# Kernel tuning notes

Measured on AMD Instinct MI355X. Metric: run time of the kernel, lower is better.

The kernel has to match this reference:

```python
import jax, jax.numpy as jnp
import numpy as np

SFREQ = 250.0
L_FREQ, H_FREQ = 4.0, 8.0
N_TAPS = 413  # odd, zero-phase FIR


def _bandpass_fir(numtaps, lf, hf, sfreq):
    # Hamming-windowed sinc band-pass (firwin-style), matching MNE's fir_design='firwin' spirit
    n = np.arange(numtaps) - (numtaps - 1) / 2.0
    lp = lambda fc: (2.0 * fc / sfreq) * np.sinc(2.0 * fc / sfreq * n)
    h = (lp(hf) - lp(lf)) * np.hamming(numtaps)
    return h.astype(np.float32)


def setup_inputs() -> dict:
    key = jax.random.key(0)
    x = jax.random.normal(key, (64, 64, 10000), dtype=jnp.float32)
    h = jnp.asarray(_bandpass_fir(N_TAPS, L_FREQ, H_FREQ, SFREQ))
    return {"x": x, "h": h}


def reference(x, h):
    # x: [B, C, T], h: [n_h] FIR filter. Equivalent math to _overlap_add_filter:
    # reflect_limited padding + full linear FFT convolution + zero-phase crop.
    T = x.shape[-1]
    n_h = h.shape[0]
    n_edge = min(n_h, T) - 1
    # reflect_limited pad: 2*x[0] - x[n_edge:0:-1] (left), 2*x[-1] - x[-2:-n_edge-2:-1] (right)
    left = 2.0 * x[..., :1] - x[..., 1:n_edge + 1][..., ::-1]
    right = 2.0 * x[..., -1:] - x[..., -n_edge - 1:-1][..., ::-1]
    x_ext = jnp.concatenate([left, x, right], axis=-1)  # [B, C, T + 2*n_edge]
    n_x = T + 2 * n_edge
    n_full = n_x + n_h - 1
    n_fft = 1 << (n_full - 1).bit_length()  # single big FFT == overlap-add result
    Xf = jnp.fft.rfft(x_ext, n_fft)
    Hf = jnp.fft.rfft(h.astype(x_ext.dtype), n_fft)
    y = jnp.fft.irfft(Xf * Hf, n_fft)  # full linear convolution of x_ext with h
    shift = (n_h - 1) // 2 + n_edge  # zero-phase delay compensation + edge crop
    return jax.lax.dynamic_slice_in_dim(y, shift, T, axis=-1).astype(x.dtype)
```

## Files before the change

kernel.cpp:

```cpp
#include <hip/hip_runtime.h>


#define T_LEN 10000
#define N_H   413
#define SHIFT 206
#define CB    512
#define BSPAN 3584
#define ROWH  936
#define NQ    28
#define AROWL 472

typedef _Float16 v8h   __attribute__((ext_vector_type(8)));
typedef float    v16f  __attribute__((ext_vector_type(16)));
typedef float    v4f   __attribute__((ext_vector_type(4)));
typedef float    f32x2 __attribute__((ext_vector_type(2)));

__device__ __forceinline__ void stage_load(const float* __restrict__ xr, int t0s,
                                           int jt, float sv[4][16]) {
    #pragma unroll
    for (int it = 0; it < 4; ++it) {
        const int c = jt + 16 * it;
        if (c < 58) {
            const int j0 = t0s + 16 * c;
            if (j0 >= SHIFT && j0 + 16 <= T_LEN + SHIFT) {
                const f32x2* xp = (const f32x2*)(xr + (j0 - SHIFT));
                #pragma unroll
                for (int p = 0; p < 8; ++p) {
                    f32x2 t2 = xp[p]; sv[it][2*p] = t2.x; sv[it][2*p+1] = t2.y;
                }
            } else {
                #pragma unroll
                for (int k = 0; k < 16; ++k) {
                    const int j = j0 + k;
                    float v;
                    if (j < SHIFT)              v = 2.0f * xr[0] - xr[SHIFT - j];
                    else if (j < T_LEN + SHIFT) v = xr[j - SHIFT];
                    else                        v = 2.0f * xr[T_LEN - 1] - xr[2 * T_LEN + SHIFT - 2 - j];
                    sv[it][k] = v;
                }
            }
        }
    }
}

__device__ __forceinline__ void stage_write(_Float16* __restrict__ erow, int jt,
                                            const float sv[4][16]) {
    #pragma unroll
    for (int it = 0; it < 4; ++it) {
        const int c = jt + 16 * it;
        if (c < 58) {
            v8h h0, h1;
            #pragma unroll
            for (int k = 0; k < 8; ++k) {
                h0[k] = (_Float16)sv[it][k]; h1[k] = (_Float16)sv[it][8 + k];
            }
            *(v8h*)(erow + 16 * c)     = h0;
            *(v8h*)(erow + 16 * c + 8) = h1;
        }
    }
}

__device__ __forceinline__ void store_col(float* __restrict__ orow, const v16f& acc,
                                          int tbase, int guard_needed) {
    #pragma unroll
    for (int g = 0; g < 4; ++g) {
        if (!guard_needed || (tbase + 8 * g) < T_LEN) {
            *(v4f*)(orow + 8 * g) =
                (v4f){acc[4*g], acc[4*g+1], acc[4*g+2], acc[4*g+3]};
        }
    }
}

__global__ __launch_bounds__(256, 3) void FilterBank_20624432955781_kernel(
    const float* __restrict__ x, const float* __restrict__ h, float* __restrict__ out) {
    __shared__ alignas(16) _Float16 lds_e[16 * ROWH];
    __shared__ alignas(16) _Float16 arow[2][8][AROWL];

    const int tid    = threadIdx.x;
    const int t_base = blockIdx.x * BSPAN;
    const int r0     = blockIdx.y * 16;
    const int nseg   = min(7, (T_LEN - t_base + CB - 1) / CB);

    for (int z = tid; z < 8 * AROWL; z += 256) {
        const int r = z / AROWL, vv = z - r * AROWL;
        const int idx = 436 + r - vv;
        const float gv = (idx >= 0 && idx < N_H) ? h[idx] : 0.0f;
        const _Float16 hi = (_Float16)gv;
        arow[0][r][vv] = hi;
        arow[1][r][vv] = (_Float16)(gv - (float)hi);
    }

    const int rr = tid >> 4;
    const int jt = tid & 15;
    const float* __restrict__ xr = x + (size_t)(r0 + rr) * T_LEN;
    _Float16* __restrict__ erow = lds_e + rr * ROWH;

    float sv[4][16];
    stage_load(xr, t_base, jt, sv);
    stage_write(erow, jt, sv);
    __syncthreads();

    const int l  = tid & 63;
    const int wv = tid >> 6;
    const int n  = l & 31;
    const int hh = l >> 5;
    const int ch = n & 15;
    const int th = n >> 4;
    const int vv0 = 24 + 8 * hh - 8 * (n >> 3);
    const v8h* __restrict__ pah = (const v8h*)(&arow[0][n & 7][0] + vv0);
    const v8h* __restrict__ pal = (const v8h*)(&arow[1][n & 7][0] + vv0);
    const _Float16* __restrict__ ebase = lds_e + ch * ROWH + 32 * th + 8 * hh;
    const _Float16* __restrict__ eb0 = ebase + 64 * wv;
    const _Float16* __restrict__ eb1 = ebase + 64 * (wv + 4);
    float* __restrict__ orow = out + (size_t)(r0 + ch) * T_LEN;

    for (int s = 0; s < nseg; ++s) {
        const int t0s = t_base + s * CB;

        if (s + 1 < nseg) stage_load(xr, t0s + CB, jt, sv);

        __builtin_amdgcn_s_setprio(1);
        v16f acc0 = (v16f)(0.0f), acc1 = (v16f)(0.0f);
        #pragma unroll
        for (int q = 0; q < NQ; ++q) {
            const v8h ah = pah[2 * q];
            const v8h al = pal[2 * q];
            const v8h b0 = *(const v8h*)(eb0 + 16 * q);
            const v8h b1 = *(const v8h*)(eb1 + 16 * q);
            acc0 = __builtin_amdgcn_mfma_f32_32x32x16_f16(ah, b0, acc0, 0, 0, 0);
            acc1 = __builtin_amdgcn_mfma_f32_32x32x16_f16(ah, b1, acc1, 0, 0, 0);
            acc0 = __builtin_amdgcn_mfma_f32_32x32x16_f16(al, b0, acc0, 0, 0, 0);
            acc1 = __builtin_amdgcn_mfma_f32_32x32x16_f16(al, b1, acc1, 0, 0, 0);
        }
        __builtin_amdgcn_s_setprio(0);

        const int guard = (t0s + CB > T_LEN);
        const int tb0 = t0s + 64 * wv + 32 * th + 4 * hh;
        store_col(orow + tb0, acc0, tb0, guard);
        store_col(orow + tb0 + 256, acc1, tb0 + 256, guard);

        if (s + 1 < nseg) {
            __syncthreads();
            stage_write(erow, jt, sv);
            __syncthreads();
        }
    }
}

extern "C" void kernel_launch(void* const* d_in, const int* in_sizes, int n_in,
                              void* d_out, int out_size, void* d_ws, size_t ws_size,
                              hipStream_t stream) {
    const float* x = (const float*)d_in[0];
    const float* h = (const float*)d_in[1];
    float* out = (float*)d_out;
    dim3 grid(3, 64 * 64 / 16);
    FilterBank_20624432955781_kernel<<<grid, dim3(256), 0, stream>>>(x, h, out);
}
```

Baseline: 334.5 us.

## Retile FIR MFMA to 8 channels per block with wider time chunks

Each block now handles 8 channels by 1024-sample chunks, where before it handled 16 channels by 512 samples. Grid and LDS staging change to match, and occupancy rises to 4 blocks per CU. Wave tiles whose second accumulator would fall past the end of the signal now skip that MFMA chain, which cuts padding work in the tail. Output stores are moved after the LDS restage so they overlap with the barrier. The tradeoff is less reuse of the filter coefficients across channels per block and higher register pressure per thread under the tighter launch bound.

```diff
diff --git a/kernel.cpp b/kernel.cpp
--- a/kernel.cpp
+++ b/kernel.cpp
@@ -4,9 +4,10 @@
 #define T_LEN 10000
 #define N_H   413
 #define SHIFT 206
-#define CB    512
-#define BSPAN 3584
-#define ROWH  936
+#define CB    1024
+#define BSPAN 5120
+#define ROWH  1480
+#define NCHK  92
 #define NQ    28
 #define AROWL 472
 
@@ -16,11 +17,11 @@
 typedef float    f32x2 __attribute__((ext_vector_type(2)));
 
 __device__ __forceinline__ void stage_load(const float* __restrict__ xr, int t0s,
-                                           int jt, float sv[4][16]) {
+                                           int jt, float sv[3][16]) {
     #pragma unroll
-    for (int it = 0; it < 4; ++it) {
-        const int c = jt + 16 * it;
-        if (c < 58) {
+    for (int it = 0; it < 3; ++it) {
+        const int c = jt + 32 * it;
+        if (c < NCHK) {
             const int j0 = t0s + 16 * c;
             if (j0 >= SHIFT && j0 + 16 <= T_LEN + SHIFT) {
                 const f32x2* xp = (const f32x2*)(xr + (j0 - SHIFT));
@@ -44,11 +45,11 @@
 }
 
 __device__ __forceinline__ void stage_write(_Float16* __restrict__ erow, int jt,
-                                            const float sv[4][16]) {
+                                            const float sv[3][16]) {
     #pragma unroll
-    for (int it = 0; it < 4; ++it) {
-        const int c = jt + 16 * it;
-        if (c < 58) {
+    for (int it = 0; it < 3; ++it) {
+        const int c = jt + 32 * it;
+        if (c < NCHK) {
             v8h h0, h1;
             #pragma unroll
             for (int k = 0; k < 8; ++k) {
@@ -71,15 +72,15 @@
     }
 }
 
-__global__ __launch_bounds__(256, 3) void FilterBank_20624432955781_kernel(
+__global__ __launch_bounds__(256, 4) void FilterBank_20624432955781_kernel(
     const float* __restrict__ x, const float* __restrict__ h, float* __restrict__ out) {
-    __shared__ alignas(16) _Float16 lds_e[16 * ROWH];
+    __shared__ alignas(16) _Float16 lds_e[8 * ROWH];
     __shared__ alignas(16) _Float16 arow[2][8][AROWL];
 
     const int tid    = threadIdx.x;
     const int t_base = blockIdx.x * BSPAN;
-    const int r0     = blockIdx.y * 16;
-    const int nseg   = min(7, (T_LEN - t_base + CB - 1) / CB);
+    const int r0     = blockIdx.y * 8;
+    const int nseg   = (min(BSPAN, T_LEN - t_base) + CB - 1) / CB;
 
     for (int z = tid; z < 8 * AROWL; z += 256) {
         const int r = z / AROWL, vv = z - r * AROWL;
@@ -90,12 +91,12 @@
         arow[1][r][vv] = (_Float16)(gv - (float)hi);
     }
 
-    const int rr = tid >> 4;
-    const int jt = tid & 15;
+    const int rr = tid >> 5;
+    const int jt = tid & 31;
     const float* __restrict__ xr = x + (size_t)(r0 + rr) * T_LEN;
     _Float16* __restrict__ erow = lds_e + rr * ROWH;
 
-    float sv[4][16];
+    float sv[3][16];
     stage_load(xr, t_base, jt, sv);
     stage_write(erow, jt, sv);
     __syncthreads();
@@ -104,46 +105,66 @@
     const int wv = tid >> 6;
     const int n  = l & 31;
     const int hh = l >> 5;
-    const int ch = n & 15;
-    const int th = n >> 4;
-    const int vv0 = 24 + 8 * hh - 8 * (n >> 3);
+    const int ch = n & 7;
+    const int tq = n >> 3;
+    const int vv0 = 24 + 8 * hh - 8 * tq;
     const v8h* __restrict__ pah = (const v8h*)(&arow[0][n & 7][0] + vv0);
     const v8h* __restrict__ pal = (const v8h*)(&arow[1][n & 7][0] + vv0);
-    const _Float16* __restrict__ ebase = lds_e + ch * ROWH + 32 * th + 8 * hh;
-    const _Float16* __restrict__ eb0 = ebase + 64 * wv;
-    const _Float16* __restrict__ eb1 = ebase + 64 * (wv + 4);
+    const _Float16* __restrict__ ebase = lds_e + ch * ROWH + 32 * tq + 8 * hh;
+    const _Float16* __restrict__ eb0 = ebase + 128 * wv;
+    const _Float16* __restrict__ eb1 = ebase + 128 * (wv + 4);
     float* __restrict__ orow = out + (size_t)(r0 + ch) * T_LEN;
 
     for (int s = 0; s < nseg; ++s) {
         const int t0s = t_base + s * CB;
+        const int last = (s + 1 == nseg);
 
-        if (s + 1 < nseg) stage_load(xr, t0s + CB, jt, sv);
+        if (!last) stage_load(xr, t0s + CB, jt, sv);
+
+        const int NQd = min(8, (T_LEN - t0s + 127) >> 7);
+        const int dual = (wv + 4 < NQd);
 
         __builtin_amdgcn_s_setprio(1);
         v16f acc0 = (v16f)(0.0f), acc1 = (v16f)(0.0f);
-        #pragma unroll
-        for (int q = 0; q < NQ; ++q) {
-            const v8h ah = pah[2 * q];
-            const v8h al = pal[2 * q];
-            const v8h b0 = *(const v8h*)(eb0 + 16 * q);
-            const v8h b1 = *(const v8h*)(eb1 + 16 * q);
-            acc0 = __builtin_amdgcn_mfma_f32_32x32x16_f16(ah, b0, acc0, 0, 0, 0);
-            acc1 = __builtin_amdgcn_mfma_f32_32x32x16_f16(ah, b1, acc1, 0, 0, 0);
-            acc0 = __builtin_amdgcn_mfma_f32_32x32x16_f16(al, b0, acc0, 0, 0, 0);
-            acc1 = __builtin_amdgcn_mfma_f32_32x32x16_f16(al, b1, acc1, 0, 0, 0);
+        if (dual) {
+            #pragma unroll
+            for (int q = 0; q < NQ; ++q) {
+                const v8h ah = pah[2 * q];
+                const v8h al = pal[2 * q];
+                const v8h b0 = *(const v8h*)(eb0 + 16 * q);
+                const v8h b1 = *(const v8h*)(eb1 + 16 * q);
+                acc0 = __builtin_amdgcn_mfma_f32_32x32x16_f16(ah, b0, acc0, 0, 0, 0);
+                acc1 = __builtin_amdgcn_mfma_f32_32x32x16_f16(ah, b1, acc1, 0, 0, 0);
+                acc0 = __builtin_amdgcn_mfma_f32_32x32x16_f16(al, b0, acc0, 0, 0, 0);
+                acc1 = __builtin_amdgcn_mfma_f32_32x32x16_f16(al, b1, acc1, 0, 0, 0);
+            }
+        } else {
+            #pragma unroll
+            for (int q = 0; q < NQ; ++q) {
+                const v8h ah = pah[2 * q];
+                const v8h al = pal[2 * q];
+                const v8h b0 = *(const v8h*)(eb0 + 16 * q);
+                acc0 = __builtin_amdgcn_mfma_f32_32x32x16_f16(ah, b0, acc0, 0, 0, 0);
+                acc0 = __builtin_amdgcn_mfma_f32_32x32x16_f16(al, b0, acc0, 0, 0, 0);
+            }
         }
         __builtin_amdgcn_s_setprio(0);
 
-        const int guard = (t0s + CB > T_LEN);
-        const int tb0 = t0s + 64 * wv + 32 * th + 4 * hh;
-        store_col(orow + tb0, acc0, tb0, guard);
-        store_col(orow + tb0 + 256, acc1, tb0 + 256, guard);
-
-        if (s + 1 < nseg) {
+        if (!last) {
             __syncthreads();
             stage_write(erow, jt, sv);
-            __syncthreads();
         }
+
+        {
+            const int tb0 = t0s + 128 * wv + 32 * tq + 4 * hh;
+            store_col(orow + tb0, acc0, tb0, (t0s + 128 * wv + 128) > T_LEN);
+            if (dual) {
+                const int tb1 = tb0 + 512;
+                store_col(orow + tb1, acc1, tb1, (t0s + 128 * (wv + 4) + 128) > T_LEN);
+            }
+        }
+
+        if (!last) __syncthreads();
     }
 }
 
@@ -153,6 +174,6 @@
     const float* x = (const float*)d_in[0];
     const float* h = (const float*)d_in[1];
     float* out = (float*)d_out;
-    dim3 grid(3, 64 * 64 / 16);
+    dim3 grid(2, 64 * 64 / 8);
     FilterBank_20624432955781_kernel<<<grid, dim3(256), 0, stream>>>(x, h, out);
 }
```

After: 314.9 us. 5.9% less time.
